# Optimization experiments

Hardware: AMD Instinct MI355X
Metric: run time of the kernel (lower is better)

## Reference

```python
import jax, jax.numpy as jnp
import numpy as np
import math

DEPTH = 1024
B, SQ, SKV = 4, 2048, 2048


def setup_inputs() -> dict:
    key = jax.random.key(0)
    ks = jax.random.split(key, 12)
    s = 1.0 / math.sqrt(DEPTH)
    inp = {
        "input": jax.random.normal(ks[0], (B, SQ, DEPTH), jnp.float32),
        "memory": jax.random.normal(ks[1], (B, SKV, DEPTH), jnp.float32),
        "mask": jax.random.randint(ks[2], (B, SQ, SKV), 0, 2, jnp.int32),
        "Wq": jax.random.uniform(ks[3], (DEPTH, DEPTH), jnp.float32, -s, s),
        "bq": jax.random.uniform(ks[4], (DEPTH,), jnp.float32, -s, s),
        "Wk": jax.random.uniform(ks[5], (DEPTH, DEPTH), jnp.float32, -s, s),
        "bk": jax.random.uniform(ks[6], (DEPTH,), jnp.float32, -s, s),
        "Wv": jax.random.uniform(ks[7], (DEPTH, DEPTH), jnp.float32, -s, s),
        "bv": jax.random.uniform(ks[8], (DEPTH,), jnp.float32, -s, s),
        "Wo": jax.random.uniform(ks[9], (DEPTH, DEPTH), jnp.float32, -s, s),
        "bo": jax.random.uniform(ks[10], (DEPTH,), jnp.float32, -s, s),
    }
    return inp


def reference(input, memory, mask, Wq, bq, Wk, bk, Wv, bv, Wo, bo):
    # torch Linear: y = x @ W.T + b
    q = jnp.einsum("bsd,ed->bse", input, Wq) + bq    # [B,SQ,D]
    k = jnp.einsum("bsd,ed->bse", memory, Wk) + bk   # [B,SKV,D]
    v = jnp.einsum("bsd,ed->bse", memory, Wv) + bv   # [B,SKV,D]
    scale = 1.0 / math.sqrt(DEPTH)
    scores = jnp.einsum("bqd,bkd->bqk", q, k) * scale  # [B,SQ,SKV]
    scores = jnp.where(mask == 0, jnp.float32(-1e10), scores)
    attn = jax.nn.softmax(scores, axis=-1)
    ctx = jnp.einsum("bqk,bkd->bqd", attn, v)
    out = jnp.einsum("bqd,ed->bqe", ctx, Wo) + bo
    return out
```

## Files before the change

kernel.cpp:

```cpp
#include <hip/hip_runtime.h>
#include <hip/hip_bf16.h>
#include <math.h>

#define NB 4
#define NSQ 2048
#define NSKV 2048
#define ND 1024

typedef __attribute__((ext_vector_type(8))) __bf16 bf16x8;
typedef __attribute__((ext_vector_type(4))) float f32x4;

__device__ __forceinline__ unsigned short f2bf(float x) {
  __hip_bfloat16 h = __float2bfloat16(x);
  return __builtin_bit_cast(unsigned short, h);
}

__device__ __forceinline__ void gload_lds16(const void* g, void* l) {
  __builtin_amdgcn_global_load_lds((const __attribute__((address_space(1))) void*)g,
                                   (__attribute__((address_space(3))) void*)l,
                                   16, 0, 0);
}

__global__ __launch_bounds__(256) void cvt_bf16(const float* __restrict__ s,
                                                unsigned short* __restrict__ d,
                                                int n4) {
  int i = blockIdx.x * blockDim.x + threadIdx.x;
  if (i >= n4) return;
  float4 v = ((const float4*)s)[i];
  ushort4 o;
  o.x = f2bf(v.x); o.y = f2bf(v.y); o.z = f2bf(v.z); o.w = f2bf(v.w);
  ((ushort4*)d)[i] = o;
}

template <int BIAS_MODE, int OUT_BF16>
__global__ __launch_bounds__(256)
void gemm_nt(const unsigned short* __restrict__ A,
             const unsigned short* __restrict__ B,
             const float* __restrict__ bias, float scale,
             void* __restrict__ Cout,
             int K, int lda, int ldb, int ldc,
             long strideA, long strideB, long strideC) {
  __shared__ __align__(16) unsigned short sA[128 * 32];
  __shared__ __align__(16) unsigned short sB[128 * 32];
  const int tid = threadIdx.x;
  const int wave = tid >> 6;
  const int lane = tid & 63;
  const long brow = (long)blockIdx.y * 128;
  const long bcol = (long)blockIdx.x * 128;
  const unsigned short* Ab = A + (long)blockIdx.z * strideA;
  const unsigned short* Bb = B + (long)blockIdx.z * strideB;

  const int wr = wave >> 1;
  const int wc = wave & 1;

  f32x4 acc[4][4];
#pragma unroll
  for (int m = 0; m < 4; ++m)
#pragma unroll
    for (int n = 0; n < 4; ++n) {
      f32x4 z = {0.f, 0.f, 0.f, 0.f};
      acc[m][n] = z;
    }

  const int c0 = wave * 64 + lane;
  const int c1 = c0 + 256;
  const unsigned short* agp0 = Ab + (brow + (c0 >> 2)) * (long)lda + (c0 & 3) * 8;
  const unsigned short* agp1 = Ab + (brow + (c1 >> 2)) * (long)lda + (c1 & 3) * 8;
  const unsigned short* bgp0 = Bb + (bcol + (c0 >> 2)) * (long)ldb + (c0 & 3) * 8;
  const unsigned short* bgp1 = Bb + (bcol + (c1 >> 2)) * (long)ldb + (c1 & 3) * 8;
  unsigned short* la0 = sA + wave * 512;
  unsigned short* la1 = sA + wave * 512 + 2048;
  unsigned short* lb0 = sB + wave * 512;
  unsigned short* lb1 = sB + wave * 512 + 2048;

  const int fr = lane & 15;
  const int ko = (lane >> 4) * 8;
  const int nk = K >> 5;

  for (int kt = 0; kt < nk; ++kt) {
    gload_lds16(agp0, la0);
    gload_lds16(agp1, la1);
    gload_lds16(bgp0, lb0);
    gload_lds16(bgp1, lb1);
    agp0 += 32; agp1 += 32; bgp0 += 32; bgp1 += 32;
    __syncthreads();

    bf16x8 af[4], bfr[4];
#pragma unroll
    for (int m = 0; m < 4; ++m)
      af[m] = *(const bf16x8*)(sA + (wr * 64 + m * 16 + fr) * 32 + ko);
#pragma unroll
    for (int n = 0; n < 4; ++n)
      bfr[n] = *(const bf16x8*)(sB + (wc * 64 + n * 16 + fr) * 32 + ko);
#pragma unroll
    for (int m = 0; m < 4; ++m)
#pragma unroll
      for (int n = 0; n < 4; ++n)
        acc[m][n] = __builtin_amdgcn_mfma_f32_16x16x32_bf16(af[m], bfr[n], acc[m][n], 0, 0, 0);
    __syncthreads();
  }

  const int fq = lane >> 4;
#pragma unroll
  for (int m = 0; m < 4; ++m) {
#pragma unroll
    for (int n = 0; n < 4; ++n) {
#pragma unroll
      for (int r = 0; r < 4; ++r) {
        long row = brow + wr * 64 + m * 16 + fq * 4 + r;
        long col = bcol + wc * 64 + n * 16 + fr;
        float v = acc[m][n][r] * scale;
        if (BIAS_MODE == 1) v += bias[col];
        if (BIAS_MODE == 2) v += bias[row];
        long idx = (long)blockIdx.z * strideC + row * (long)ldc + col;
        if (OUT_BF16)
          ((unsigned short*)Cout)[idx] = f2bf(v);
        else
          ((float*)Cout)[idx] = v;
      }
    }
  }
}

__global__ __launch_bounds__(256)
void softmax_mask(const float* __restrict__ S, const int* __restrict__ Mk,
                  unsigned short* __restrict__ P) {
  const long row = blockIdx.x;
  const float* s = S + row * NSKV;
  const int* mk = Mk + row * NSKV;
  unsigned short* p = P + row * NSKV;
  const int t = threadIdx.x;
  const int lane = t & 63;
  const int wave = t >> 6;

  float4 v0 = ((const float4*)s)[t * 2];
  float4 v1 = ((const float4*)s)[t * 2 + 1];
  int4 m0 = ((const int4*)mk)[t * 2];
  int4 m1 = ((const int4*)mk)[t * 2 + 1];
  float x[8];
  x[0] = m0.x ? v0.x : -1e10f;
  x[1] = m0.y ? v0.y : -1e10f;
  x[2] = m0.z ? v0.z : -1e10f;
  x[3] = m0.w ? v0.w : -1e10f;
  x[4] = m1.x ? v1.x : -1e10f;
  x[5] = m1.y ? v1.y : -1e10f;
  x[6] = m1.z ? v1.z : -1e10f;
  x[7] = m1.w ? v1.w : -1e10f;

  float mx = x[0];
#pragma unroll
  for (int j = 1; j < 8; ++j) mx = fmaxf(mx, x[j]);
#pragma unroll
  for (int o = 32; o > 0; o >>= 1) mx = fmaxf(mx, __shfl_xor(mx, o, 64));
  __shared__ float red[8];
  if (lane == 0) red[wave] = mx;
  __syncthreads();
  mx = fmaxf(fmaxf(red[0], red[1]), fmaxf(red[2], red[3]));

  float e[8];
  float sum = 0.f;
#pragma unroll
  for (int j = 0; j < 8; ++j) {
    e[j] = __expf(x[j] - mx);
    sum += e[j];
  }
#pragma unroll
  for (int o = 32; o > 0; o >>= 1) sum += __shfl_xor(sum, o, 64);
  if (lane == 0) red[4 + wave] = sum;
  __syncthreads();
  sum = red[4] + red[5] + red[6] + red[7];
  float inv = 1.f / sum;

  ushort4 o0, o1;
  o0.x = f2bf(e[0] * inv); o0.y = f2bf(e[1] * inv);
  o0.z = f2bf(e[2] * inv); o0.w = f2bf(e[3] * inv);
  o1.x = f2bf(e[4] * inv); o1.y = f2bf(e[5] * inv);
  o1.z = f2bf(e[6] * inv); o1.w = f2bf(e[7] * inv);
  ((ushort4*)p)[t * 2] = o0;
  ((ushort4*)p)[t * 2 + 1] = o1;
}

extern "C" void kernel_launch(void* const* d_in, const int* in_sizes, int n_in,
                              void* d_out, int out_size, void* d_ws, size_t ws_size,
                              hipStream_t stream) {
  const float* input  = (const float*)d_in[0];
  const float* memory = (const float*)d_in[1];
  const int*   mask   = (const int*)d_in[2];
  const float* Wq = (const float*)d_in[3];
  const float* bq = (const float*)d_in[4];
  const float* Wk = (const float*)d_in[5];
  const float* bk = (const float*)d_in[6];
  const float* Wv = (const float*)d_in[7];
  const float* bv = (const float*)d_in[8];
  const float* Wo = (const float*)d_in[9];
  const float* bo = (const float*)d_in[10];
  float* out = (float*)d_out;

  unsigned short* wqb  = (unsigned short*)d_ws;
  unsigned short* wkb  = wqb + (1 << 20);
  unsigned short* wvb  = wkb + (1 << 20);
  unsigned short* wob  = wvb + (1 << 20);
  unsigned short* inb  = wob + (1 << 20);
  unsigned short* memb = inb + (8 << 20);
  unsigned short* qb   = memb + (8 << 20);
  unsigned short* kb   = qb + (8 << 20);
  unsigned short* vtb  = kb + (8 << 20);
  unsigned short* ctxb = vtb + (8 << 20);
  float* scoresf = (float*)(ctxb + (8 << 20));
  unsigned short* pb = inb;

  cvt_bf16<<<dim3(8192), 256, 0, stream>>>(input, inb, 2097152);
  cvt_bf16<<<dim3(8192), 256, 0, stream>>>(memory, memb, 2097152);
  cvt_bf16<<<dim3(1024), 256, 0, stream>>>(Wq, wqb, 262144);
  cvt_bf16<<<dim3(1024), 256, 0, stream>>>(Wk, wkb, 262144);
  cvt_bf16<<<dim3(1024), 256, 0, stream>>>(Wv, wvb, 262144);
  cvt_bf16<<<dim3(1024), 256, 0, stream>>>(Wo, wob, 262144);

  gemm_nt<1, 1><<<dim3(8, 64, 1), 256, 0, stream>>>(
      inb, wqb, bq, 1.f, qb, ND, ND, ND, ND, 0, 0, 0);
  gemm_nt<1, 1><<<dim3(8, 64, 1), 256, 0, stream>>>(
      memb, wkb, bk, 1.f, kb, ND, ND, ND, ND, 0, 0, 0);
  gemm_nt<2, 1><<<dim3(64, 8, 1), 256, 0, stream>>>(
      wvb, memb, bv, 1.f, vtb, ND, ND, ND, 8192, 0, 0, 0);
  gemm_nt<0, 0><<<dim3(16, 16, 4), 256, 0, stream>>>(
      qb, kb, nullptr, 0.03125f, scoresf, ND, ND, ND, NSKV,
      (long)NSQ * ND, (long)NSKV * ND, (long)NSQ * NSKV);
  softmax_mask<<<dim3(NB * NSQ), 256, 0, stream>>>(scoresf, mask, pb);
  gemm_nt<0, 1><<<dim3(8, 16, 4), 256, 0, stream>>>(
      pb, vtb, nullptr, 1.f, ctxb, NSKV, NSKV, 8192, ND,
      (long)NSQ * NSKV, (long)NSKV, (long)NSQ * ND);
  gemm_nt<1, 0><<<dim3(8, 64, 1), 256, 0, stream>>>(
      ctxb, wob, bo, 1.f, out, ND, ND, ND, ND, 0, 0, 0);
}
```

Measured before the change: 440.4 us.

## Replace 128x128 GEMM with 256x256 double-buffered swizzled 8-wave kernel and batch Q/K projections

```diff
diff --git a/kernel.cpp b/kernel.cpp
--- a/kernel.cpp
+++ b/kernel.cpp
@@ -9,6 +9,10 @@
 
 typedef __attribute__((ext_vector_type(8))) __bf16 bf16x8;
 typedef __attribute__((ext_vector_type(4))) float f32x4;
+
+#define WAITV(N) asm volatile("s_waitcnt vmcnt(" #N ")" ::: "memory")
+#define WAITL0() asm volatile("s_waitcnt lgkmcnt(0)" ::: "memory")
+#define BAR() __builtin_amdgcn_s_barrier()
 
 __device__ __forceinline__ unsigned short f2bf(float x) {
   __hip_bfloat16 h = __float2bfloat16(x);
@@ -32,86 +36,179 @@
   ((ushort4*)d)[i] = o;
 }
 
+__global__ __launch_bounds__(256) void concat_bias(const float* __restrict__ a,
+                                                   const float* __restrict__ b,
+                                                   float* __restrict__ d) {
+  int i = blockIdx.x * 256 + threadIdx.x;
+  if (i < 1024) d[i] = a[i];
+  else if (i < 2048) d[i] = b[i - 1024];
+}
+
 template <int BIAS_MODE, int OUT_BF16>
-__global__ __launch_bounds__(256)
-void gemm_nt(const unsigned short* __restrict__ A,
+__global__ __launch_bounds__(512)
+void gemm256(const unsigned short* __restrict__ A,
              const unsigned short* __restrict__ B,
-             const float* __restrict__ bias, float scale,
+             const float* __restrict__ bias, int biasStride, float scale,
              void* __restrict__ Cout,
              int K, int lda, int ldb, int ldc,
              long strideA, long strideB, long strideC) {
-  __shared__ __align__(16) unsigned short sA[128 * 32];
-  __shared__ __align__(16) unsigned short sB[128 * 32];
+  extern __shared__ __align__(16) char smem[];
+  char* ldsA = smem;
+  char* ldsB = smem + 65536;
+
   const int tid = threadIdx.x;
-  const int wave = tid >> 6;
-  const int lane = tid & 63;
-  const long brow = (long)blockIdx.y * 128;
-  const long bcol = (long)blockIdx.x * 128;
+  const int w  = tid >> 6;
+  const int l  = tid & 63;
+  const int wm = w >> 2;
+  const int wn = w & 3;
+  const int fr = l & 15;
+  const int fq = l >> 4;
+
+  const long brow = (long)blockIdx.y * 256;
+  const long bcol = (long)blockIdx.x * 256;
   const unsigned short* Ab = A + (long)blockIdx.z * strideA;
   const unsigned short* Bb = B + (long)blockIdx.z * strideB;
-
-  const int wr = wave >> 1;
-  const int wc = wave & 1;
-
-  f32x4 acc[4][4];
-#pragma unroll
-  for (int m = 0; m < 4; ++m)
-#pragma unroll
-    for (int n = 0; n < 4; ++n) {
+  const float* biasb = (BIAS_MODE ? bias + (long)blockIdx.z * (long)biasStride : nullptr);
+
+  const int NT = K >> 6;
+
+  int srow[2], skc[2];
+#pragma unroll
+  for (int r = 0; r < 2; ++r) {
+    int c = r * 512 + w * 64 + l;
+    srow[r] = c >> 3;
+    skc[r] = ((c & 7) - srow[r]) & 7;
+  }
+  const int sldsoff0 = (w * 64) * 16;
+  const int sldsoff1 = (512 + w * 64) * 16;
+
+  auto STAGE = [&](int isB, int T, int h) {
+    const unsigned short* Gb = isB ? Bb : Ab;
+    const int ld = isB ? ldb : lda;
+    const long rb = (isB ? bcol : brow) + h * 128;
+    char* seg = (isB ? ldsB : ldsA) + (T & 1) * 32768 + h * 16384;
+    gload_lds16(Gb + (rb + srow[0]) * (long)ld + T * 64 + skc[0] * 8, seg + sldsoff0);
+    gload_lds16(Gb + (rb + srow[1]) * (long)ld + T * 64 + skc[1] * 8, seg + sldsoff1);
+  };
+
+  auto LDFRAG = [&](const char* seg, int row, int kc) -> bf16x8 {
+    return *(const bf16x8*)(seg + row * 128 + (((kc + row) & 7) << 4));
+  };
+
+  f32x4 acc[8][4];
+#pragma unroll
+  for (int mi = 0; mi < 8; ++mi)
+#pragma unroll
+    for (int ni = 0; ni < 4; ++ni) {
       f32x4 z = {0.f, 0.f, 0.f, 0.f};
-      acc[m][n] = z;
+      acc[mi][ni] = z;
     }
 
-  const int c0 = wave * 64 + lane;
-  const int c1 = c0 + 256;
-  const unsigned short* agp0 = Ab + (brow + (c0 >> 2)) * (long)lda + (c0 & 3) * 8;
-  const unsigned short* agp1 = Ab + (brow + (c1 >> 2)) * (long)lda + (c1 & 3) * 8;
-  const unsigned short* bgp0 = Bb + (bcol + (c0 >> 2)) * (long)ldb + (c0 & 3) * 8;
-  const unsigned short* bgp1 = Bb + (bcol + (c1 >> 2)) * (long)ldb + (c1 & 3) * 8;
-  unsigned short* la0 = sA + wave * 512;
-  unsigned short* la1 = sA + wave * 512 + 2048;
-  unsigned short* lb0 = sB + wave * 512;
-  unsigned short* lb1 = sB + wave * 512 + 2048;
-
-  const int fr = lane & 15;
-  const int ko = (lane >> 4) * 8;
-  const int nk = K >> 5;
-
-  for (int kt = 0; kt < nk; ++kt) {
-    gload_lds16(agp0, la0);
-    gload_lds16(agp1, la1);
-    gload_lds16(bgp0, lb0);
-    gload_lds16(bgp1, lb1);
-    agp0 += 32; agp1 += 32; bgp0 += 32; bgp1 += 32;
-    __syncthreads();
-
-    bf16x8 af[4], bfr[4];
-#pragma unroll
-    for (int m = 0; m < 4; ++m)
-      af[m] = *(const bf16x8*)(sA + (wr * 64 + m * 16 + fr) * 32 + ko);
-#pragma unroll
-    for (int n = 0; n < 4; ++n)
-      bfr[n] = *(const bf16x8*)(sB + (wc * 64 + n * 16 + fr) * 32 + ko);
-#pragma unroll
-    for (int m = 0; m < 4; ++m)
-#pragma unroll
-      for (int n = 0; n < 4; ++n)
-        acc[m][n] = __builtin_amdgcn_mfma_f32_16x16x32_bf16(af[m], bfr[n], acc[m][n], 0, 0, 0);
-    __syncthreads();
+  bf16x8 af[4][2], bfr[2][2];
+
+  STAGE(0, 0, 0); STAGE(1, 0, 0); STAGE(1, 0, 1); STAGE(0, 0, 1);
+  WAITV(4);
+  STAGE(0, 1, 0); STAGE(1, 1, 1); STAGE(0, 1, 1);
+  WAITV(6);
+  BAR();
+
+  for (int t = 0; t < NT; ++t) {
+    const int cb = t & 1;
+    const char* a0 = ldsA + cb * 32768;
+    const char* a1 = a0 + 16384;
+    const char* b0 = ldsB + cb * 32768;
+    const char* b1 = b0 + 16384;
+
+#pragma unroll
+    for (int mi = 0; mi < 4; ++mi)
+#pragma unroll
+      for (int ks = 0; ks < 2; ++ks)
+        af[mi][ks] = LDFRAG(a0, wm * 64 + mi * 16 + fr, ks * 4 + fq);
+#pragma unroll
+    for (int ni = 0; ni < 2; ++ni)
+#pragma unroll
+      for (int ks = 0; ks < 2; ++ks)
+        bfr[ni][ks] = LDFRAG(b0, wn * 32 + ni * 16 + fr, ks * 4 + fq);
+    if (t + 1 < NT) STAGE(1, t + 1, 0);
+    BAR(); WAITL0();
+    __builtin_amdgcn_s_setprio(1);
+#pragma unroll
+    for (int ks = 0; ks < 2; ++ks)
+#pragma unroll
+      for (int mi = 0; mi < 4; ++mi)
+#pragma unroll
+        for (int ni = 0; ni < 2; ++ni)
+          acc[mi][ni] = __builtin_amdgcn_mfma_f32_16x16x32_bf16(af[mi][ks], bfr[ni][ks], acc[mi][ni], 0, 0, 0);
+    __builtin_amdgcn_s_setprio(0);
+    BAR();
+
+#pragma unroll
+    for (int ni = 0; ni < 2; ++ni)
+#pragma unroll
+      for (int ks = 0; ks < 2; ++ks)
+        bfr[ni][ks] = LDFRAG(b1, wn * 32 + ni * 16 + fr, ks * 4 + fq);
+    if (t + 2 < NT) STAGE(0, t + 2, 0);
+    BAR(); WAITL0();
+    __builtin_amdgcn_s_setprio(1);
+#pragma unroll
+    for (int ks = 0; ks < 2; ++ks)
+#pragma unroll
+      for (int mi = 0; mi < 4; ++mi)
+#pragma unroll
+        for (int ni = 0; ni < 2; ++ni)
+          acc[mi][2 + ni] = __builtin_amdgcn_mfma_f32_16x16x32_bf16(af[mi][ks], bfr[ni][ks], acc[mi][2 + ni], 0, 0, 0);
+    __builtin_amdgcn_s_setprio(0);
+    BAR();
+
+#pragma unroll
+    for (int mi = 0; mi < 4; ++mi)
+#pragma unroll
+      for (int ks = 0; ks < 2; ++ks)
+        af[mi][ks] = LDFRAG(a1, wm * 64 + mi * 16 + fr, ks * 4 + fq);
+    if (t + 2 < NT) STAGE(1, t + 2, 1);
+    BAR(); WAITL0();
+    __builtin_amdgcn_s_setprio(1);
+#pragma unroll
+    for (int ks = 0; ks < 2; ++ks)
+#pragma unroll
+      for (int mi = 0; mi < 4; ++mi)
+#pragma unroll
+        for (int ni = 0; ni < 2; ++ni)
+          acc[4 + mi][2 + ni] = __builtin_amdgcn_mfma_f32_16x16x32_bf16(af[mi][ks], bfr[ni][ks], acc[4 + mi][2 + ni], 0, 0, 0);
+    __builtin_amdgcn_s_setprio(0);
+    BAR();
+
+#pragma unroll
+    for (int ni = 0; ni < 2; ++ni)
+#pragma unroll
+      for (int ks = 0; ks < 2; ++ks)
+        bfr[ni][ks] = LDFRAG(b0, wn * 32 + ni * 16 + fr, ks * 4 + fq);
+    if (t + 2 < NT) STAGE(0, t + 2, 1);
+    BAR(); WAITL0();
+    __builtin_amdgcn_s_setprio(1);
+#pragma unroll
+    for (int ks = 0; ks < 2; ++ks)
+#pragma unroll
+      for (int mi = 0; mi < 4; ++mi)
+#pragma unroll
+        for (int ni = 0; ni < 2; ++ni)
+          acc[4 + mi][ni] = __builtin_amdgcn_mfma_f32_16x16x32_bf16(af[mi][ks], bfr[ni][ks], acc[4 + mi][ni], 0, 0, 0);
+    __builtin_amdgcn_s_setprio(0);
+    if (t < NT - 2) { WAITV(6); } else if (t == NT - 2) { WAITV(0); }
+    BAR();
   }
 
-  const int fq = lane >> 4;
-#pragma unroll
-  for (int m = 0; m < 4; ++m) {
-#pragma unroll
-    for (int n = 0; n < 4; ++n) {
+#pragma unroll
+  for (int mi = 0; mi < 8; ++mi) {
+#pragma unroll
+    for (int ni = 0; ni < 4; ++ni) {
 #pragma unroll
       for (int r = 0; r < 4; ++r) {
-        long row = brow + wr * 64 + m * 16 + fq * 4 + r;
-        long col = bcol + wc * 64 + n * 16 + fr;
-        float v = acc[m][n][r] * scale;
-        if (BIAS_MODE == 1) v += bias[col];
-        if (BIAS_MODE == 2) v += bias[row];
+        long row = brow + (mi >> 2) * 128 + wm * 64 + (mi & 3) * 16 + fq * 4 + r;
+        long col = bcol + (ni >> 1) * 128 + wn * 32 + (ni & 1) * 16 + fr;
+        float v = acc[mi][ni][r] * scale;
+        if (BIAS_MODE == 1) v += biasb[col];
+        if (BIAS_MODE == 2) v += biasb[row];
         long idx = (long)blockIdx.z * strideC + row * (long)ldc + col;
         if (OUT_BF16)
           ((unsigned short*)Cout)[idx] = f2bf(v);
@@ -207,7 +304,15 @@
   unsigned short* vtb  = kb + (8 << 20);
   unsigned short* ctxb = vtb + (8 << 20);
   float* scoresf = (float*)(ctxb + (8 << 20));
+  float* biasqk  = scoresf + (16 << 20);
   unsigned short* pb = inb;
+
+  const int SMEM = 131072;
+  hipFuncSetAttribute((const void*)&gemm256<1, 1>, hipFuncAttributeMaxDynamicSharedMemorySize, SMEM);
+  hipFuncSetAttribute((const void*)&gemm256<2, 1>, hipFuncAttributeMaxDynamicSharedMemorySize, SMEM);
+  hipFuncSetAttribute((const void*)&gemm256<0, 0>, hipFuncAttributeMaxDynamicSharedMemorySize, SMEM);
+  hipFuncSetAttribute((const void*)&gemm256<0, 1>, hipFuncAttributeMaxDynamicSharedMemorySize, SMEM);
+  hipFuncSetAttribute((const void*)&gemm256<1, 0>, hipFuncAttributeMaxDynamicSharedMemorySize, SMEM);
 
   cvt_bf16<<<dim3(8192), 256, 0, stream>>>(input, inb, 2097152);
   cvt_bf16<<<dim3(8192), 256, 0, stream>>>(memory, memb, 2097152);
@@ -215,20 +320,20 @@
   cvt_bf16<<<dim3(1024), 256, 0, stream>>>(Wk, wkb, 262144);
   cvt_bf16<<<dim3(1024), 256, 0, stream>>>(Wv, wvb, 262144);
   cvt_bf16<<<dim3(1024), 256, 0, stream>>>(Wo, wob, 262144);
-
-  gemm_nt<1, 1><<<dim3(8, 64, 1), 256, 0, stream>>>(
-      inb, wqb, bq, 1.f, qb, ND, ND, ND, ND, 0, 0, 0);
-  gemm_nt<1, 1><<<dim3(8, 64, 1), 256, 0, stream>>>(
-      memb, wkb, bk, 1.f, kb, ND, ND, ND, ND, 0, 0, 0);
-  gemm_nt<2, 1><<<dim3(64, 8, 1), 256, 0, stream>>>(
-      wvb, memb, bv, 1.f, vtb, ND, ND, ND, 8192, 0, 0, 0);
-  gemm_nt<0, 0><<<dim3(16, 16, 4), 256, 0, stream>>>(
-      qb, kb, nullptr, 0.03125f, scoresf, ND, ND, ND, NSKV,
+  concat_bias<<<dim3(8), 256, 0, stream>>>(bq, bk, biasqk);
+
+  gemm256<1, 1><<<dim3(4, 32, 2), 512, SMEM, stream>>>(
+      inb, wqb, biasqk, 1024, 1.f, qb, ND, ND, ND, ND,
+      (long)(8 << 20), (long)(1 << 20), (long)(8 << 20));
+  gemm256<2, 1><<<dim3(32, 4, 1), 512, SMEM, stream>>>(
+      wvb, memb, bv, 0, 1.f, vtb, ND, ND, ND, 8192, 0, 0, 0);
+  gemm256<0, 0><<<dim3(8, 8, 4), 512, SMEM, stream>>>(
+      qb, kb, nullptr, 0, 0.03125f, scoresf, ND, ND, ND, NSKV,
       (long)NSQ * ND, (long)NSKV * ND, (long)NSQ * NSKV);
   softmax_mask<<<dim3(NB * NSQ), 256, 0, stream>>>(scoresf, mask, pb);
-  gemm_nt<0, 1><<<dim3(8, 16, 4), 256, 0, stream>>>(
-      pb, vtb, nullptr, 1.f, ctxb, NSKV, NSKV, 8192, ND,
+  gemm256<0, 1><<<dim3(4, 8, 4), 512, SMEM, stream>>>(
+      pb, vtb, nullptr, 0, 1.f, ctxb, NSKV, NSKV, 8192, ND,
       (long)NSQ * NSKV, (long)NSKV, (long)NSQ * ND);
-  gemm_nt<1, 0><<<dim3(8, 64, 1), 256, 0, stream>>>(
-      ctxb, wob, bo, 1.f, out, ND, ND, ND, ND, 0, 0, 0);
-}
+  gemm256<1, 0><<<dim3(4, 32, 1), 512, SMEM, stream>>>(
+      ctxb, wob, bo, 0, 1.f, out, ND, ND, ND, ND, 0, 0, 0);
+}
```

After: 397.1 us. 9.8% less time.
